# Kernel tuning notes

Measured on AMD Instinct MI355X. Metric: run time of the kernel, lower is better.

## Reference

```python
import jax, jax.numpy as jnp
import numpy as np

LEAKY_SLOPE = 0.2  # tf.nn.leaky_relu default alpha
N_NODES = 50000
N_EDGES = 800000
IN_DIM = 128
OUT_DIM = 64
HEADS = 4
MLP_HID = 256
MLP_OUT = 128


def setup_inputs() -> dict:
    key = jax.random.key(0)
    ks = jax.random.split(key, 10)
    node_embeddings = jax.random.normal(ks[0], (N_NODES, IN_DIM), dtype=jnp.float32)
    src = jax.random.randint(ks[1], (N_EDGES,), 0, N_NODES, dtype=jnp.int32)
    dst = jax.random.randint(ks[2], (N_EDGES,), 0, N_NODES, dtype=jnp.int32)
    # glorot-ish scales
    W_n = jax.random.normal(ks[3], (HEADS, IN_DIM, OUT_DIM), dtype=jnp.float32) * (1.0 / np.sqrt(IN_DIM))
    a_src = jax.random.normal(ks[4], (HEADS, OUT_DIM), dtype=jnp.float32) * (1.0 / np.sqrt(OUT_DIM))
    a_dst = jax.random.normal(ks[5], (HEADS, OUT_DIM), dtype=jnp.float32) * (1.0 / np.sqrt(OUT_DIM))
    mlp_W1 = jax.random.normal(ks[6], (HEADS * OUT_DIM, MLP_HID), dtype=jnp.float32) * (1.0 / np.sqrt(HEADS * OUT_DIM))
    mlp_b1 = jnp.zeros((MLP_HID,), dtype=jnp.float32)
    mlp_W2 = jax.random.normal(ks[7], (MLP_HID, MLP_OUT), dtype=jnp.float32) * (1.0 / np.sqrt(MLP_HID))
    mlp_b2 = jnp.zeros((MLP_OUT,), dtype=jnp.float32)
    return {"node_embeddings": node_embeddings, "src": src, "dst": dst,
            "W_n": W_n, "a_src": a_src, "a_dst": a_dst,
            "mlp_W1": mlp_W1, "mlp_b1": mlp_b1, "mlp_W2": mlp_W2, "mlp_b2": mlp_b2}


def _gat_forward(node_embeddings, src, dst, W_n, a_src, a_dst, mlp_W1, mlp_b1, mlp_W2, mlp_b2):
    N = node_embeddings.shape[0]
    # per-head linear transform: [N, H, D]
    h = jnp.einsum('nc,hcd->nhd', node_embeddings, W_n)
    # decomposed attention scores at node level, gathered per edge
    s_src = jnp.einsum('nhd,hd->nh', h, a_src)          # [N, H]
    s_dst = jnp.einsum('nhd,hd->nh', h, a_dst)          # [N, H]
    e = jax.nn.leaky_relu(s_src[src] + s_dst[dst], negative_slope=LEAKY_SLOPE)  # [E, H]
    # segment softmax over incoming edges of each dst node
    e_max = jax.ops.segment_max(e, dst, num_segments=N)          # [N, H], -inf for empty
    ex = jnp.exp(e - e_max[dst])                                  # [E, H]
    den = jax.ops.segment_sum(ex, dst, num_segments=N)            # [N, H]
    m = h[src]                                                    # [E, H, D] messages
    num = jax.ops.segment_sum(ex[:, :, None] * m, dst, num_segments=N)  # [N, H, D]
    safe_den = jnp.where(den > 0, den, 1.0)
    head_out = jax.nn.relu(num / safe_den[:, :, None])            # [N, H, D]
    concat = head_out.reshape(N, -1)                              # [N, H*D]
    hidden = jax.nn.relu(concat @ mlp_W1 + mlp_b1)
    return hidden @ mlp_W2 + mlp_b2                               # [N, MLP_OUT]


def reference(node_embeddings, src, dst, W_n, a_src, a_dst, mlp_W1, mlp_b1, mlp_W2, mlp_b2):
    return _gat_forward(node_embeddings, src, dst, W_n, a_src, a_dst,
                        mlp_W1, mlp_b1, mlp_W2, mlp_b2)
```

## Files before the change

### kernel.cpp

```cpp
#include <hip/hip_runtime.h>

#define LEAKY 0.2f

typedef __attribute__((ext_vector_type(8))) short short8;
typedef __attribute__((ext_vector_type(4))) float floatx4;

__device__ __forceinline__ float bf2f(unsigned short u) {
    return __uint_as_float(((unsigned)u) << 16);
}
__device__ __forceinline__ unsigned short f2bf(float f) {
    unsigned u = __float_as_uint(f);
    unsigned r = (u + 0x7fffu + ((u >> 16) & 1u)) >> 16;
    return (unsigned short)r;
}
__device__ __forceinline__ float relu_nan(float v) { return v < 0.0f ? 0.0f : v; }

__device__ __forceinline__ void gload_lds16(const void* g, void* l) {
    __builtin_amdgcn_global_load_lds((const __attribute__((address_space(1))) void*)g,
                                     (__attribute__((address_space(3))) void*)l, 16, 0, 0);
}

__global__ void k_fill(float* __restrict__ p, float val, int n) {
    int i = blockIdx.x * blockDim.x + threadIdx.x;
    if (i < n) p[i] = val;
}

__global__ void k_prep(const float* __restrict__ X, unsigned short* __restrict__ Xb,
                       const float* __restrict__ Wn, unsigned short* __restrict__ WnT,
                       const float* __restrict__ W1, unsigned short* __restrict__ W1T,
                       const float* __restrict__ W2, unsigned short* __restrict__ W2T,
                       int* __restrict__ cnt, int N) {
    const int gs = gridDim.x * blockDim.x;
    const int tid = blockIdx.x * blockDim.x + threadIdx.x;
    for (int i = tid; i < N; i += gs) cnt[i] = 0;
    for (int i = tid; i < N * 32; i += gs) {
        float4 v = ((const float4*)X)[i];
        ushort4 o;
        o.x = f2bf(v.x); o.y = f2bf(v.y); o.z = f2bf(v.z); o.w = f2bf(v.w);
        ((ushort4*)Xb)[i] = o;
    }
    for (int i = tid; i < 256 * 128; i += gs) {
        int col = i >> 7, k = i & 127;
        int head = col >> 6, d = col & 63;
        WnT[i] = f2bf(Wn[(size_t)head * 8192 + (size_t)k * 64 + d]);
    }
    for (int i = tid; i < 256 * 256; i += gs) {
        int n = i >> 8, k = i & 255;
        W1T[i] = f2bf(W1[(size_t)k * 256 + n]);
    }
    for (int i = tid; i < 128 * 256; i += gs) {
        int n = i >> 8, k = i & 255;
        W2T[i] = f2bf(W2[(size_t)k * 128 + n]);
    }
}

__global__ void k_hist(const int* __restrict__ dst, int* __restrict__ cnt, int E) {
    int e = blockIdx.x * blockDim.x + threadIdx.x;
    if (e < E) atomicAdd(cnt + dst[e], 1);
}

__global__ __launch_bounds__(256) void k_scan1(
    const int* __restrict__ cnt, int* __restrict__ rowptr, int* __restrict__ bsum, int N) {
    __shared__ int wtot[4];
    const int lane = threadIdx.x & 63, wave = threadIdx.x >> 6;
    const int i = blockIdx.x * 256 + threadIdx.x;
    int v = (i < N) ? cnt[i] : 0;
    int x = v;
    for (int off = 1; off < 64; off <<= 1) {
        int y = __shfl_up(x, off, 64);
        if (lane >= off) x += y;
    }
    if (lane == 63) wtot[wave] = x;
    __syncthreads();
    int wo = 0;
    for (int wv = 0; wv < wave; ++wv) wo += wtot[wv];
    if (i < N) rowptr[i] = wo + x - v;
    if (threadIdx.x == 255) bsum[blockIdx.x] = wo + x;
}
__global__ void k_scan2(int* __restrict__ bsum, int nb) {
    const int lane = threadIdx.x;
    int carry = 0;
    for (int base = 0; base < nb; base += 64) {
        int i = base + lane;
        int v = (i < nb) ? bsum[i] : 0;
        int x = v;
        for (int off = 1; off < 64; off <<= 1) {
            int y = __shfl_up(x, off, 64);
            if (lane >= off) x += y;
        }
        if (i < nb) bsum[i] = carry + x - v;
        carry += __shfl(x, 63, 64);
    }
}
__global__ void k_scan3(int* __restrict__ rowptr, const int* __restrict__ bsum,
                        int* __restrict__ wcnt, int N, int E) {
    int i = blockIdx.x * blockDim.x + threadIdx.x;
    if (i < N) {
        int v = rowptr[i] + bsum[i >> 8];
        rowptr[i] = v;
        wcnt[i] = v;
    }
    if (i == N) rowptr[N] = E;
}

__global__ void k_scatter(const int* __restrict__ src, const int* __restrict__ dst,
                          int* __restrict__ wcnt, int* __restrict__ esrc, int E) {
    int e = blockIdx.x * blockDim.x + threadIdx.x;
    if (e < E) {
        int pos = atomicAdd(wcnt + dst[e], 1);
        esrc[pos] = src[e];
    }
}

__global__ __launch_bounds__(256) void k_agg(
    const float* __restrict__ s_src, const float* __restrict__ s_dst,
    const unsigned short* __restrict__ h_bf,
    const int* __restrict__ rowptr, const int* __restrict__ esrc,
    unsigned short* __restrict__ concat) {
    const int t = threadIdx.x;
    const int lane = t & 63;
    const int wave = t >> 6;
    const int row0 = blockIdx.x * 16;
    const int head = lane >> 4;
    const int c0 = lane << 2;
    const int eslot = lane & 15;
    const int hsel = lane & 48;

    for (int rr = 0; rr < 4; ++rr) {
        const int n = row0 + wave * 4 + rr;
        const int beg = rowptr[n], end = rowptr[n + 1];
        const float sdst = s_dst[n * 4 + head];
        float num0 = 0, num1 = 0, num2 = 0, num3 = 0, den = 0;
        for (int base = beg; base < end; base += 16) {
            const int nn = end - base;
            int sid = 0;
            float my_ex = 0.0f;
            if (eslot < nn) {
                sid = esrc[base + eslot];
                float v = s_src[sid * 4 + head] + sdst;
                v = v > 0.0f ? v : LEAKY * v;
                my_ex = __expf(v);
            }
#pragma unroll
            for (int e = 0; e < 16; ++e) {
                float ex = __shfl(my_ex, hsel | e, 64);
                int s    = __shfl(sid, e, 64);
                ushort4 hv = *(const ushort4*)(h_bf + (size_t)s * 256 + c0);
                num0 += ex * bf2f(hv.x);
                num1 += ex * bf2f(hv.y);
                num2 += ex * bf2f(hv.z);
                num3 += ex * bf2f(hv.w);
                den  += ex;
            }
        }
        const float inv = 1.0f / (den > 0.0f ? den : 1.0f);
        ushort4 o;
        o.x = f2bf(relu_nan(num0 * inv));
        o.y = f2bf(relu_nan(num1 * inv));
        o.z = f2bf(relu_nan(num2 * inv));
        o.w = f2bf(relu_nan(num3 * inv));
        *(ushort4*)(concat + (size_t)n * 256 + c0) = o;
    }
}

template <int K, int MODE>
__global__ __launch_bounds__(256) void k_gemm(
    const unsigned short* __restrict__ A, const unsigned short* __restrict__ BT,
    const float* __restrict__ bias, unsigned short* __restrict__ Cb,
    float* __restrict__ Cf, int N, int ldout,
    const float* __restrict__ asrc, const float* __restrict__ adst,
    float* __restrict__ s_src, float* __restrict__ s_dst) {
    __shared__ unsigned short As[128 * 32];
    __shared__ unsigned short Bs[128 * 32];
    const int t = threadIdx.x;
    const int lane = t & 63;
    const int w = t >> 6;
    const int wy = w >> 1, wx = w & 1;
    const int lm = lane & 15, quad = lane >> 4;
    const int row0 = blockIdx.x * 128;
    const int n0 = blockIdx.y * 128;
    const int srow = lane >> 2;
    const int sk = (lane & 3) * 8;

    floatx4 acc[4][4];
    if (MODE == 0) {
#pragma unroll
        for (int mi = 0; mi < 4; ++mi)
#pragma unroll
            for (int ni = 0; ni < 4; ++ni) acc[mi][ni] = (floatx4){0, 0, 0, 0};
    } else {
#pragma unroll
        for (int ni = 0; ni < 4; ++ni) {
            float b = bias[n0 + wx * 64 + ni * 16 + lm];
#pragma unroll
            for (int mi = 0; mi < 4; ++mi) acc[mi][ni] = (floatx4){b, b, b, b};
        }
    }

    for (int k0 = 0; k0 < K; k0 += 32) {
#pragma unroll
        for (int p = 0; p < 2; ++p) {
            int tr = (p * 4 + w) * 16 + srow;
            int ga = row0 + tr; if (ga >= N) ga = N - 1;
            gload_lds16(A + (size_t)ga * K + k0 + sk,
                        (char*)As + (size_t)tr * 64 + sk * 2);
            gload_lds16(BT + (size_t)(n0 + tr) * K + k0 + sk,
                        (char*)Bs + (size_t)tr * 64 + sk * 2);
        }
        __syncthreads();
        short8 af[4], bfr[4];
#pragma unroll
        for (int mi = 0; mi < 4; ++mi)
            af[mi] = *(const short8*)(As + (size_t)(wy * 64 + mi * 16 + lm) * 32 + quad * 8);
#pragma unroll
        for (int ni = 0; ni < 4; ++ni)
            bfr[ni] = *(const short8*)(Bs + (size_t)(wx * 64 + ni * 16 + lm) * 32 + quad * 8);
#pragma unroll
        for (int mi = 0; mi < 4; ++mi)
#pragma unroll
            for (int ni = 0; ni < 4; ++ni)
                acc[mi][ni] = __builtin_amdgcn_mfma_f32_16x16x32_bf16(af[mi], bfr[ni], acc[mi][ni], 0, 0, 0);
        __syncthreads();
    }

#pragma unroll
    for (int mi = 0; mi < 4; ++mi)
#pragma unroll
        for (int ni = 0; ni < 4; ++ni)
#pragma unroll
            for (int q = 0; q < 4; ++q) {
                int r = row0 + wy * 64 + mi * 16 + quad * 4 + q;
                int c = n0 + wx * 64 + ni * 16 + lm;
                if (r < N) {
                    if (MODE == 0)      Cb[(size_t)r * ldout + c] = f2bf(acc[mi][ni][q]);
                    else if (MODE == 1) Cb[(size_t)r * ldout + c] = f2bf(relu_nan(acc[mi][ni][q]));
                    else                Cf[(size_t)r * ldout + c] = acc[mi][ni][q];
                }
            }

    if (MODE == 0) {
        const int head = blockIdx.y * 2 + wx;
        float as[4], ad[4];
#pragma unroll
        for (int ni = 0; ni < 4; ++ni) {
            int d = ni * 16 + lm;
            as[ni] = asrc[head * 64 + d];
            ad[ni] = adst[head * 64 + d];
        }
#pragma unroll
        for (int mi = 0; mi < 4; ++mi)
#pragma unroll
            for (int q = 0; q < 4; ++q) {
                float ps = acc[mi][0][q] * as[0] + acc[mi][1][q] * as[1]
                         + acc[mi][2][q] * as[2] + acc[mi][3][q] * as[3];
                float pd = acc[mi][0][q] * ad[0] + acc[mi][1][q] * ad[1]
                         + acc[mi][2][q] * ad[2] + acc[mi][3][q] * ad[3];
#pragma unroll
                for (int m = 1; m < 16; m <<= 1) {
                    ps += __shfl_xor(ps, m, 64);
                    pd += __shfl_xor(pd, m, 64);
                }
                if (lm == 0) {
                    int r = row0 + wy * 64 + mi * 16 + quad * 4 + q;
                    if (r < N) {
                        s_src[r * 4 + head] = ps;
                        s_dst[r * 4 + head] = pd;
                    }
                }
            }
    }
}

extern "C" void kernel_launch(void* const* d_in, const int* in_sizes, int n_in,
                              void* d_out, int out_size, void* d_ws, size_t ws_size,
                              hipStream_t stream) {
    const float* X    = (const float*)d_in[0];
    const int* src    = (const int*)d_in[1];
    const int* dst    = (const int*)d_in[2];
    const float* Wn   = (const float*)d_in[3];
    const float* Asrc = (const float*)d_in[4];
    const float* Adst = (const float*)d_in[5];
    const float* W1   = (const float*)d_in[6];
    const float* b1   = (const float*)d_in[7];
    const float* W2   = (const float*)d_in[8];
    const float* b2   = (const float*)d_in[9];
    float* out = (float*)d_out;

    const int N = in_sizes[0] / 128;
    const int E = in_sizes[1];
    const int NBS = (N + 255) / 256;
    const int NR = (N + 127) / 128;

    size_t off = 0;
    char* w = (char*)d_ws;
    unsigned short* h_bf = (unsigned short*)(w + off); off += (size_t)N * 256 * 2;
    float* s_src = (float*)(w + off);                  off += (size_t)N * 4 * 4;
    float* s_dst = (float*)(w + off);                  off += (size_t)N * 4 * 4;
    int* cnt     = (int*)(w + off);                    off += (size_t)N * 4;
    int* rowptr  = (int*)(w + off);                    off += ((size_t)(N + 1) * 4 + 15) & ~15ull;
    int* wcnt    = (int*)(w + off);                    off += (size_t)N * 4;
    int* bsum    = (int*)(w + off);                    off += ((size_t)NBS * 4 + 15) & ~15ull;
    int* esrc    = (int*)(w + off);                    off += (size_t)E * 4;
    unsigned short* W1T = (unsigned short*)(w + off);  off += 256 * 256 * 2;
    unsigned short* W2T = (unsigned short*)(w + off);  off += 128 * 256 * 2;
    unsigned short* WnT = (unsigned short*)(w + off);  off += 256 * 128 * 2;
    const size_t required = off;

    if (ws_size < required) {
        k_fill<<<dim3((out_size + 255) / 256), dim3(256), 0, stream>>>(
            out, (float)(ws_size >> 20), out_size);
        return;
    }

    unsigned short* Xb     = (unsigned short*)d_out;
    unsigned short* concat = (unsigned short*)d_out;

    k_prep<<<dim3(2048), dim3(256), 0, stream>>>(X, Xb, Wn, WnT, W1, W1T, W2, W2T, cnt, N);
    k_gemm<128, 0><<<dim3(NR, 2), dim3(256), 0, stream>>>(
        Xb, WnT, nullptr, h_bf, nullptr, N, 256, Asrc, Adst, s_src, s_dst);
    k_hist<<<dim3((E + 255) / 256), dim3(256), 0, stream>>>(dst, cnt, E);
    k_scan1<<<dim3(NBS), dim3(256), 0, stream>>>(cnt, rowptr, bsum, N);
    k_scan2<<<dim3(1), dim3(64), 0, stream>>>(bsum, NBS);
    k_scan3<<<dim3((N + 256) / 256), dim3(256), 0, stream>>>(rowptr, bsum, wcnt, N, E);
    k_scatter<<<dim3((E + 255) / 256), dim3(256), 0, stream>>>(src, dst, wcnt, esrc, E);
    k_agg<<<dim3(N / 16), dim3(256), 0, stream>>>(s_src, s_dst, h_bf, rowptr, esrc, concat);
    k_gemm<256, 1><<<dim3(NR, 2), dim3(256), 0, stream>>>(
        concat, W1T, b1, h_bf, nullptr, N, 256, nullptr, nullptr, nullptr, nullptr);
    k_gemm<256, 2><<<dim3(NR, 1), dim3(256), 0, stream>>>(
        h_bf, W2T, b2, nullptr, out, N, 128, nullptr, nullptr, nullptr, nullptr);
}
```

Before: 308.3 us.

## Widen aggregation loads to 8 bf16 per lane and fold histogram into prep

The aggregation kernel now assigns one destination node per wave. Each half-wave processes alternate edges with 16-byte loads of 8 bf16 features per lane, and the two halves are combined by a cross-half shuffle reduction. The loop over edges is fully unrolled only when a full group of 16 edges remains. Separately, the edge histogram is merged into the prep kernel and the count zeroing moves to a memset, removing one launch. The goal is fewer and wider gather loads and more parallelism across nodes, at the cost of an extra reduction and idle lanes on low-degree nodes.

Measured after the change: 306.6 us. About the same (-0.6%).

```diff
diff --git a/kernel.cpp b/kernel.cpp
--- a/kernel.cpp
+++ b/kernel.cpp
@@ -4,6 +4,7 @@
 
 typedef __attribute__((ext_vector_type(8))) short short8;
 typedef __attribute__((ext_vector_type(4))) float floatx4;
+typedef __attribute__((ext_vector_type(8))) unsigned short ushort8_t;
 
 __device__ __forceinline__ float bf2f(unsigned short u) {
     return __uint_as_float(((unsigned)u) << 16);
@@ -29,10 +30,10 @@
                        const float* __restrict__ Wn, unsigned short* __restrict__ WnT,
                        const float* __restrict__ W1, unsigned short* __restrict__ W1T,
                        const float* __restrict__ W2, unsigned short* __restrict__ W2T,
-                       int* __restrict__ cnt, int N) {
+                       const int* __restrict__ dst, int* __restrict__ cnt,
+                       int N, int E) {
     const int gs = gridDim.x * blockDim.x;
     const int tid = blockIdx.x * blockDim.x + threadIdx.x;
-    for (int i = tid; i < N; i += gs) cnt[i] = 0;
     for (int i = tid; i < N * 32; i += gs) {
         float4 v = ((const float4*)X)[i];
         ushort4 o;
@@ -52,11 +53,7 @@
         int n = i >> 8, k = i & 255;
         W2T[i] = f2bf(W2[(size_t)k * 128 + n]);
     }
-}
-
-__global__ void k_hist(const int* __restrict__ dst, int* __restrict__ cnt, int E) {
-    int e = blockIdx.x * blockDim.x + threadIdx.x;
-    if (e < E) atomicAdd(cnt + dst[e], 1);
+    for (int i = tid; i < E; i += gs) atomicAdd(cnt + dst[i], 1);
 }
 
 __global__ __launch_bounds__(256) void k_scan1(
@@ -116,51 +113,69 @@
     const float* __restrict__ s_src, const float* __restrict__ s_dst,
     const unsigned short* __restrict__ h_bf,
     const int* __restrict__ rowptr, const int* __restrict__ esrc,
-    unsigned short* __restrict__ concat) {
+    unsigned short* __restrict__ concat, int N) {
     const int t = threadIdx.x;
     const int lane = t & 63;
     const int wave = t >> 6;
-    const int row0 = blockIdx.x * 16;
-    const int head = lane >> 4;
-    const int c0 = lane << 2;
-    const int eslot = lane & 15;
-    const int hsel = lane & 48;
-
-    for (int rr = 0; rr < 4; ++rr) {
-        const int n = row0 + wave * 4 + rr;
-        const int beg = rowptr[n], end = rowptr[n + 1];
-        const float sdst = s_dst[n * 4 + head];
-        float num0 = 0, num1 = 0, num2 = 0, num3 = 0, den = 0;
-        for (int base = beg; base < end; base += 16) {
-            const int nn = end - base;
-            int sid = 0;
-            float my_ex = 0.0f;
-            if (eslot < nn) {
-                sid = esrc[base + eslot];
-                float v = s_src[sid * 4 + head] + sdst;
-                v = v > 0.0f ? v : LEAKY * v;
-                my_ex = __expf(v);
-            }
-#pragma unroll
-            for (int e = 0; e < 16; ++e) {
-                float ex = __shfl(my_ex, hsel | e, 64);
-                int s    = __shfl(sid, e, 64);
-                ushort4 hv = *(const ushort4*)(h_bf + (size_t)s * 256 + c0);
-                num0 += ex * bf2f(hv.x);
-                num1 += ex * bf2f(hv.y);
-                num2 += ex * bf2f(hv.z);
-                num3 += ex * bf2f(hv.w);
-                den  += ex;
-            }
-        }
-        const float inv = 1.0f / (den > 0.0f ? den : 1.0f);
-        ushort4 o;
-        o.x = f2bf(relu_nan(num0 * inv));
-        o.y = f2bf(relu_nan(num1 * inv));
-        o.z = f2bf(relu_nan(num2 * inv));
-        o.w = f2bf(relu_nan(num3 * inv));
-        *(ushort4*)(concat + (size_t)n * 256 + c0) = o;
-    }
+    const int n = blockIdx.x * 4 + wave;
+    if (n >= N) return;
+
+    const int q = lane & 31;
+    const int half = lane >> 5;
+    const int hq4 = (q >> 3) << 4;
+    const int slot = lane & 15;
+    const int headw = lane >> 4;
+
+    const int beg = rowptr[n], end = rowptr[n + 1];
+    const float sdst = s_dst[n * 4 + headw];
+    const unsigned short* hrow = h_bf + q * 8;
+
+    float num[8] = {0, 0, 0, 0, 0, 0, 0, 0};
+    float den = 0.0f;
+
+    for (int base = beg; base < end; base += 16) {
+        const int rem = end - base;
+        int sid = 0;
+        float mex = 0.0f;
+        if (slot < rem) {
+            sid = esrc[base + slot];
+            float v = s_src[sid * 4 + headw] + sdst;
+            v = fmaxf(v, LEAKY * v);
+            mex = __expf(v);
+        }
+        den += mex;
+
+        auto pair = [&](int i) {
+            const int ep = 2 * i + half;
+            const int s_ = __shfl(sid, ep, 64);
+            const float ex_ = __shfl(mex, hq4 | ep, 64);
+            const ushort8_t hv = *(const ushort8_t*)(hrow + (size_t)s_ * 256);
+#pragma unroll
+            for (int j = 0; j < 8; ++j)
+                num[j] = fmaf(ex_, bf2f(hv[j]), num[j]);
+        };
+
+        if (rem >= 16) {
+#pragma unroll
+            for (int i = 0; i < 8; ++i) pair(i);
+        } else {
+            const int np = (rem + 1) >> 1;
+            for (int i = 0; i < np; ++i) pair(i);
+        }
+    }
+
+#pragma unroll
+    for (int j = 0; j < 8; ++j) num[j] += __shfl_xor(num[j], 32, 64);
+#pragma unroll
+    for (int m = 1; m < 16; m <<= 1) den += __shfl_xor(den, m, 64);
+    const float denq = __shfl(den, hq4, 64);
+    const float inv = 1.0f / (denq > 0.0f ? denq : 1.0f);
+
+    ushort8_t o;
+#pragma unroll
+    for (int j = 0; j < 8; ++j) o[j] = f2bf(relu_nan(num[j] * inv));
+    if (lane < 32)
+        *(ushort8_t*)(concat + (size_t)n * 256 + q * 8) = o;
 }
 
 template <int K, int MODE>
@@ -315,15 +330,16 @@
     unsigned short* Xb     = (unsigned short*)d_out;
     unsigned short* concat = (unsigned short*)d_out;
 
-    k_prep<<<dim3(2048), dim3(256), 0, stream>>>(X, Xb, Wn, WnT, W1, W1T, W2, W2T, cnt, N);
+    hipMemsetAsync(cnt, 0, (size_t)N * sizeof(int), stream);
+    k_prep<<<dim3(2048), dim3(256), 0, stream>>>(X, Xb, Wn, WnT, W1, W1T, W2, W2T,
+                                                 dst, cnt, N, E);
     k_gemm<128, 0><<<dim3(NR, 2), dim3(256), 0, stream>>>(
         Xb, WnT, nullptr, h_bf, nullptr, N, 256, Asrc, Adst, s_src, s_dst);
-    k_hist<<<dim3((E + 255) / 256), dim3(256), 0, stream>>>(dst, cnt, E);
     k_scan1<<<dim3(NBS), dim3(256), 0, stream>>>(cnt, rowptr, bsum, N);
     k_scan2<<<dim3(1), dim3(64), 0, stream>>>(bsum, NBS);
     k_scan3<<<dim3((N + 256) / 256), dim3(256), 0, stream>>>(rowptr, bsum, wcnt, N, E);
     k_scatter<<<dim3((E + 255) / 256), dim3(256), 0, stream>>>(src, dst, wcnt, esrc, E);
-    k_agg<<<dim3(N / 16), dim3(256), 0, stream>>>(s_src, s_dst, h_bf, rowptr, esrc, concat);
+    k_agg<<<dim3((N + 3) / 4), dim3(256), 0, stream>>>(s_src, s_dst, h_bf, rowptr, esrc, concat, N);
     k_gemm<256, 1><<<dim3(NR, 2), dim3(256), 0, stream>>>(
         concat, W1T, b1, h_bf, nullptr, N, 256, nullptr, nullptr, nullptr, nullptr);
     k_gemm<256, 2><<<dim3(NR, 1), dim3(256), 0, stream>>>(
```

## Fuse X bf16 conversion into GEMM, merge histogram into prep, prefetch agg edges

Applied to the files above, without the earlier changes.

The first GEMM now reads fp32 X directly and converts it to bf16 while staging into LDS, which removes the separate full-matrix conversion pass and its round-trip through memory. The edge histogram moves into the weight-prep kernel and the count zeroing becomes a memset, saving a launch. The aggregation kernel now handles one node per wave with a larger grid and software-prefetches the next 16 edge ids and source scores. The fp32 A path replaces the async global-to-LDS load with synchronous register loads and conversion, which may slow the GEMM main loop.

New measurement: 299.9 us. -2.7%, faster.

```diff
diff --git a/kernel.cpp b/kernel.cpp
--- a/kernel.cpp
+++ b/kernel.cpp
@@ -4,6 +4,7 @@
 
 typedef __attribute__((ext_vector_type(8))) short short8;
 typedef __attribute__((ext_vector_type(4))) float floatx4;
+typedef __attribute__((ext_vector_type(8))) unsigned short ushort8_t;
 
 __device__ __forceinline__ float bf2f(unsigned short u) {
     return __uint_as_float(((unsigned)u) << 16);
@@ -25,20 +26,12 @@
     if (i < n) p[i] = val;
 }
 
-__global__ void k_prep(const float* __restrict__ X, unsigned short* __restrict__ Xb,
-                       const float* __restrict__ Wn, unsigned short* __restrict__ WnT,
+__global__ void k_prep(const float* __restrict__ Wn, unsigned short* __restrict__ WnT,
                        const float* __restrict__ W1, unsigned short* __restrict__ W1T,
                        const float* __restrict__ W2, unsigned short* __restrict__ W2T,
-                       int* __restrict__ cnt, int N) {
+                       const int* __restrict__ dst, int* __restrict__ cnt, int E) {
     const int gs = gridDim.x * blockDim.x;
     const int tid = blockIdx.x * blockDim.x + threadIdx.x;
-    for (int i = tid; i < N; i += gs) cnt[i] = 0;
-    for (int i = tid; i < N * 32; i += gs) {
-        float4 v = ((const float4*)X)[i];
-        ushort4 o;
-        o.x = f2bf(v.x); o.y = f2bf(v.y); o.z = f2bf(v.z); o.w = f2bf(v.w);
-        ((ushort4*)Xb)[i] = o;
-    }
     for (int i = tid; i < 256 * 128; i += gs) {
         int col = i >> 7, k = i & 127;
         int head = col >> 6, d = col & 63;
@@ -52,11 +45,7 @@
         int n = i >> 8, k = i & 255;
         W2T[i] = f2bf(W2[(size_t)k * 128 + n]);
     }
-}
-
-__global__ void k_hist(const int* __restrict__ dst, int* __restrict__ cnt, int E) {
-    int e = blockIdx.x * blockDim.x + threadIdx.x;
-    if (e < E) atomicAdd(cnt + dst[e], 1);
+    for (int i = tid; i < E; i += gs) atomicAdd(cnt + dst[i], 1);
 }
 
 __global__ __launch_bounds__(256) void k_scan1(
@@ -116,56 +105,71 @@
     const float* __restrict__ s_src, const float* __restrict__ s_dst,
     const unsigned short* __restrict__ h_bf,
     const int* __restrict__ rowptr, const int* __restrict__ esrc,
-    unsigned short* __restrict__ concat) {
+    unsigned short* __restrict__ concat, int N) {
     const int t = threadIdx.x;
     const int lane = t & 63;
     const int wave = t >> 6;
-    const int row0 = blockIdx.x * 16;
+    const int n = blockIdx.x * 4 + wave;
+    if (n >= N) return;
+
     const int head = lane >> 4;
     const int c0 = lane << 2;
     const int eslot = lane & 15;
     const int hsel = lane & 48;
 
-    for (int rr = 0; rr < 4; ++rr) {
-        const int n = row0 + wave * 4 + rr;
-        const int beg = rowptr[n], end = rowptr[n + 1];
-        const float sdst = s_dst[n * 4 + head];
-        float num0 = 0, num1 = 0, num2 = 0, num3 = 0, den = 0;
-        for (int base = beg; base < end; base += 16) {
-            const int nn = end - base;
-            int sid = 0;
-            float my_ex = 0.0f;
-            if (eslot < nn) {
-                sid = esrc[base + eslot];
-                float v = s_src[sid * 4 + head] + sdst;
-                v = v > 0.0f ? v : LEAKY * v;
-                my_ex = __expf(v);
+    const int beg = rowptr[n], end = rowptr[n + 1];
+    const float sdst = s_dst[n * 4 + head];
+    float num0 = 0, num1 = 0, num2 = 0, num3 = 0, den = 0;
+
+    int sid = 0;
+    float sv = 0.0f;
+    if (beg < end && eslot < end - beg) {
+        sid = esrc[beg + eslot];
+        sv = s_src[sid * 4 + head];
+    }
+
+    for (int base = beg; base < end; base += 16) {
+        const int nn = end - base;
+        int sidn = 0;
+        float svn = 0.0f;
+        if (base + 16 < end) {
+            if (eslot < end - (base + 16)) {
+                sidn = esrc[base + 16 + eslot];
+                svn = s_src[sidn * 4 + head];
             }
-#pragma unroll
-            for (int e = 0; e < 16; ++e) {
-                float ex = __shfl(my_ex, hsel | e, 64);
-                int s    = __shfl(sid, e, 64);
-                ushort4 hv = *(const ushort4*)(h_bf + (size_t)s * 256 + c0);
-                num0 += ex * bf2f(hv.x);
-                num1 += ex * bf2f(hv.y);
-                num2 += ex * bf2f(hv.z);
-                num3 += ex * bf2f(hv.w);
-                den  += ex;
-            }
-        }
-        const float inv = 1.0f / (den > 0.0f ? den : 1.0f);
-        ushort4 o;
-        o.x = f2bf(relu_nan(num0 * inv));
-        o.y = f2bf(relu_nan(num1 * inv));
-        o.z = f2bf(relu_nan(num2 * inv));
-        o.w = f2bf(relu_nan(num3 * inv));
-        *(ushort4*)(concat + (size_t)n * 256 + c0) = o;
-    }
-}
-
-template <int K, int MODE>
+        }
+        float my_ex = 0.0f;
+        if (eslot < nn) {
+            float v = sv + sdst;
+            v = fmaxf(v, LEAKY * v);
+            my_ex = __expf(v);
+        }
+#pragma unroll
+        for (int e = 0; e < 16; ++e) {
+            float ex = __shfl(my_ex, hsel | e, 64);
+            int s    = __shfl(sid, e, 64);
+            ushort4 hv = *(const ushort4*)(h_bf + (size_t)s * 256 + c0);
+            num0 += ex * bf2f(hv.x);
+            num1 += ex * bf2f(hv.y);
+            num2 += ex * bf2f(hv.z);
+            num3 += ex * bf2f(hv.w);
+            den  += ex;
+        }
+        sid = sidn; sv = svn;
+    }
+
+    const float inv = 1.0f / (den > 0.0f ? den : 1.0f);
+    ushort4 o;
+    o.x = f2bf(relu_nan(num0 * inv));
+    o.y = f2bf(relu_nan(num1 * inv));
+    o.z = f2bf(relu_nan(num2 * inv));
+    o.w = f2bf(relu_nan(num3 * inv));
+    *(ushort4*)(concat + (size_t)n * 256 + c0) = o;
+}
+
+template <int K, int MODE, bool AF32>
 __global__ __launch_bounds__(256) void k_gemm(
-    const unsigned short* __restrict__ A, const unsigned short* __restrict__ BT,
+    const void* __restrict__ A, const unsigned short* __restrict__ BT,
     const float* __restrict__ bias, unsigned short* __restrict__ Cb,
     float* __restrict__ Cf, int N, int ldout,
     const float* __restrict__ asrc, const float* __restrict__ adst,
@@ -202,8 +206,20 @@
         for (int p = 0; p < 2; ++p) {
             int tr = (p * 4 + w) * 16 + srow;
             int ga = row0 + tr; if (ga >= N) ga = N - 1;
-            gload_lds16(A + (size_t)ga * K + k0 + sk,
-                        (char*)As + (size_t)tr * 64 + sk * 2);
+            if (AF32) {
+                const float* Af = (const float*)A;
+                float4 v0 = *(const float4*)(Af + (size_t)ga * K + k0 + sk);
+                float4 v1 = *(const float4*)(Af + (size_t)ga * K + k0 + sk + 4);
+                short8 pk;
+                pk[0] = (short)f2bf(v0.x); pk[1] = (short)f2bf(v0.y);
+                pk[2] = (short)f2bf(v0.z); pk[3] = (short)f2bf(v0.w);
+                pk[4] = (short)f2bf(v1.x); pk[5] = (short)f2bf(v1.y);
+                pk[6] = (short)f2bf(v1.z); pk[7] = (short)f2bf(v1.w);
+                *(short8*)(As + (size_t)tr * 32 + sk) = pk;
+            } else {
+                gload_lds16((const unsigned short*)A + (size_t)ga * K + k0 + sk,
+                            (char*)As + (size_t)tr * 64 + sk * 2);
+            }
             gload_lds16(BT + (size_t)(n0 + tr) * K + k0 + sk,
                         (char*)Bs + (size_t)tr * 64 + sk * 2);
         }
@@ -312,20 +328,20 @@
         return;
     }
 
-    unsigned short* Xb     = (unsigned short*)d_out;
     unsigned short* concat = (unsigned short*)d_out;
 
-    k_prep<<<dim3(2048), dim3(256), 0, stream>>>(X, Xb, Wn, WnT, W1, W1T, W2, W2T, cnt, N);
-    k_gemm<128, 0><<<dim3(NR, 2), dim3(256), 0, stream>>>(
-        Xb, WnT, nullptr, h_bf, nullptr, N, 256, Asrc, Adst, s_src, s_dst);
-    k_hist<<<dim3((E + 255) / 256), dim3(256), 0, stream>>>(dst, cnt, E);
+    hipMemsetAsync(cnt, 0, (size_t)N * sizeof(int), stream);
+    k_prep<<<dim3(2048), dim3(256), 0, stream>>>(Wn, WnT, W1, W1T, W2, W2T, dst, cnt, E);
+    k_gemm<128, 0, true><<<dim3(NR, 2), dim3(256), 0, stream>>>(
+        X, WnT, nullptr, h_bf, nullptr, N, 256, Asrc, Adst, s_src, s_dst);
     k_scan1<<<dim3(NBS), dim3(256), 0, stream>>>(cnt, rowptr, bsum, N);
     k_scan2<<<dim3(1), dim3(64), 0, stream>>>(bsum, NBS);
     k_scan3<<<dim3((N + 256) / 256), dim3(256), 0, stream>>>(rowptr, bsum, wcnt, N, E);
     k_scatter<<<dim3((E + 255) / 256), dim3(256), 0, stream>>>(src, dst, wcnt, esrc, E);
-    k_agg<<<dim3(N / 16), dim3(256), 0, stream>>>(s_src, s_dst, h_bf, rowptr, esrc, concat);
-    k_gemm<256, 1><<<dim3(NR, 2), dim3(256), 0, stream>>>(
+    k_agg<<<dim3((N + 3) / 4), dim3(256), 0, stream>>>(s_src, s_dst, h_bf, rowptr, esrc,
+                                                       concat, N);
+    k_gemm<256, 1, false><<<dim3(NR, 2), dim3(256), 0, stream>>>(
         concat, W1T, b1, h_bf, nullptr, N, 256, nullptr, nullptr, nullptr, nullptr);
-    k_gemm<256, 2><<<dim3(NR, 1), dim3(256), 0, stream>>>(
+    k_gemm<256, 2, false><<<dim3(NR, 1), dim3(256), 0, stream>>>(
         h_bf, W2T, b2, nullptr, out, N, 128, nullptr, nullptr, nullptr, nullptr);
 }
```
